# Kernel tuning notes

Hardware: AMD Instinct MI355X
Metric: run time of the kernel (lower is better)

Reference implementation:

```python
import jax, jax.numpy as jnp
import numpy as np

EMBED_DIM = 1024
N_HEADS = 16
HEAD_DIM = EMBED_DIM // N_HEADS
B, T = 1, 4096

def setup_inputs() -> dict:
    key = jax.random.key(0)
    k1, k2, k3 = jax.random.split(key, 3)
    x = jax.random.normal(k1, (B, T, EMBED_DIM), dtype=jnp.float32)
    # match nn.Linear init scale roughly (not required for correctness testing)
    w_qkv = jax.random.normal(k2, (EMBED_DIM, 3 * EMBED_DIM), dtype=jnp.float32) * (EMBED_DIM ** -0.5)
    w_out = jax.random.normal(k3, (EMBED_DIM, EMBED_DIM), dtype=jnp.float32) * (EMBED_DIM ** -0.5)
    return {"x": x, "w_qkv": w_qkv, "w_out": w_out}

def reference(x, w_qkv, w_out):
    b, t, c = x.shape
    qkv = x @ w_qkv                                  # [B,T,3C]
    q, k, v = jnp.split(qkv, 3, axis=-1)
    # [B,T,C] -> [B,H,T,D]
    def heads(a):
        return a.reshape(b, t, N_HEADS, HEAD_DIM).transpose(0, 2, 1, 3)
    q, k, v = heads(q), heads(k), heads(v)
    scale = 1.0 / jnp.sqrt(jnp.asarray(HEAD_DIM, dtype=x.dtype))
    att = jnp.einsum('bhqd,bhkd->bhqk', q, k) * scale  # [B,H,T,T] (full matrix, as in source)
    att = jax.nn.softmax(att, axis=-1)
    y = jnp.einsum('bhqk,bhkd->bhqd', att, v)          # [B,H,T,D]
    y = y.transpose(0, 2, 1, 3).reshape(b, t, c)
    return y @ w_out
```

## Files before the change

### kernel.cpp

```cpp
#include <hip/hip_runtime.h>
#include <hip/hip_bf16.h>

#define T_SEQ 4096
#define C_DIM 1024
#define NH    16
#define HD    64
#define C3    3072

typedef __attribute__((ext_vector_type(8))) short short8;
typedef __attribute__((ext_vector_type(4))) short short4v;
typedef __attribute__((ext_vector_type(4))) float f32x4;
typedef __attribute__((ext_vector_type(16))) float f32x16;

__device__ __forceinline__ short f2bf(float f) {
  union { float f; unsigned u; } v; v.f = f;
  unsigned r = v.u + 0x7FFFu + ((v.u >> 16) & 1u);
  return (short)(r >> 16);
}

__device__ __forceinline__ unsigned cvt_pk_bf16(float lo, float hi) {
  unsigned r;
  asm volatile("v_cvt_pk_bf16_f32 %0, %1, %2" : "=v"(r) : "v"(lo), "v"(hi));
  return r;
}

__device__ __forceinline__ float exp2_fast(float x) {
  return __builtin_amdgcn_exp2f(x);
}

__device__ __forceinline__ float max_half64(float v) {
  return fmaxf(v, __shfl_xor(v, 32, 64));
}

__device__ __forceinline__ float m3(float a, float b, float c) {
  return fmaxf(fmaxf(a, b), c);
}

__device__ __forceinline__ void gld_lds16(const void* g, void* l) {
  __builtin_amdgcn_global_load_lds(
      (const __attribute__((address_space(1))) unsigned int*)g,
      (__attribute__((address_space(3))) unsigned int*)l, 16, 0, 0);
}

__global__ __launch_bounds__(256) void conv_bf16_kernel(const float* __restrict__ in,
                                                        short* __restrict__ out) {
  const size_t i = ((size_t)blockIdx.x * 256 + threadIdx.x) * 8;
  float4 v0 = *(const float4*)(in + i);
  float4 v1 = *(const float4*)(in + i + 4);
  short8 o;
  o[0] = f2bf(v0.x); o[1] = f2bf(v0.y); o[2] = f2bf(v0.z); o[3] = f2bf(v0.w);
  o[4] = f2bf(v1.x); o[5] = f2bf(v1.y); o[6] = f2bf(v1.z); o[7] = f2bf(v1.w);
  *(short8*)(out + i) = o;
}

__global__ void trans_conv2_kernel(const float* __restrict__ wq, short* __restrict__ wqT,
                                   const float* __restrict__ wo, short* __restrict__ woT) {
  const float* in;
  short* out;
  int N, bx = blockIdx.x;
  if (bx < C3 / 32) { in = wq; out = wqT; N = C3; }
  else              { in = wo; out = woT; N = C_DIM; bx -= C3 / 32; }
  const int K = C_DIM;
  __shared__ float t[32][33];
  const int n0 = bx * 32, k0 = blockIdx.y * 32;
  const int tx = threadIdx.x, ty = threadIdx.y;
  for (int i = ty; i < 32; i += 8) t[i][tx] = in[(size_t)(k0 + i) * N + n0 + tx];
  __syncthreads();
  for (int i = ty; i < 32; i += 8) out[(size_t)(n0 + i) * K + k0 + tx] = f2bf(t[tx][i]);
}

__global__ __launch_bounds__(256) void gemm_bt_kernel(const short* __restrict__ A,
                                                      const short* __restrict__ BT,
                                                      short* __restrict__ C,
                                                      short* __restrict__ vTout,
                                                      int vcol0,
                                                      int M, int N, int K) {
  __shared__ __align__(16) short As[128 * 32];
  __shared__ __align__(16) short Bs[128 * 32];
  const int tid = threadIdx.x;
  const int wid = tid >> 6;
  const int lane = tid & 63;
  const int l15 = lane & 15;
  const int l4 = lane >> 4;
  const int wr = wid >> 1;
  const int wc = wid & 1;

  const int nwg = gridDim.x * gridDim.y;
  int lin = blockIdx.y * gridDim.x + blockIdx.x;
  lin = (lin & 7) * (nwg >> 3) + (lin >> 3);
  const int bm = (lin / gridDim.x) * 128;
  const int bn = (lin % gridDim.x) * 128;

  f32x4 acc[4][4];
#pragma unroll
  for (int m = 0; m < 4; ++m)
#pragma unroll
    for (int n = 0; n < 4; ++n) acc[m][n] = (f32x4){0.f, 0.f, 0.f, 0.f};

  const int ebase = wid * 1024;
  const int e0 = ebase + lane * 8;
  const int r0 = e0 >> 5, c0 = e0 & 31;
  const int r1 = r0 + 16;

  for (int k0 = 0; k0 < K; k0 += 32) {
    __syncthreads();
    gld_lds16(A + (size_t)(bm + r0) * K + k0 + c0, As + ebase);
    gld_lds16(A + (size_t)(bm + r1) * K + k0 + c0, As + ebase + 512);
    gld_lds16(BT + (size_t)(bn + r0) * K + k0 + c0, Bs + ebase);
    gld_lds16(BT + (size_t)(bn + r1) * K + k0 + c0, Bs + ebase + 512);
    __syncthreads();

    short8 a[4], b[4];
#pragma unroll
    for (int m = 0; m < 4; ++m)
      a[m] = *(const short8*)&As[(wr * 64 + m * 16 + l15) * 32 + l4 * 8];
#pragma unroll
    for (int n = 0; n < 4; ++n)
      b[n] = *(const short8*)&Bs[(wc * 64 + n * 16 + l15) * 32 + l4 * 8];
#pragma unroll
    for (int m = 0; m < 4; ++m)
#pragma unroll
      for (int n = 0; n < 4; ++n)
        acc[m][n] = __builtin_amdgcn_mfma_f32_16x16x32_bf16(a[m], b[n], acc[m][n], 0, 0, 0);
  }

  if (bn >= vcol0) {
#pragma unroll
    for (int m = 0; m < 4; ++m) {
      const int row0 = bm + wr * 64 + m * 16 + l4 * 4;
#pragma unroll
      for (int n = 0; n < 4; ++n) {
        const int col = bn + wc * 64 + n * 16 + l15;
        short4v o;
#pragma unroll
        for (int r = 0; r < 4; ++r) o[r] = f2bf(acc[m][n][r]);
        *(short4v*)&vTout[(size_t)(col - vcol0) * M + row0] = o;
      }
    }
  } else {
#pragma unroll
    for (int m = 0; m < 4; ++m) {
      const int row0 = bm + wr * 64 + m * 16 + l4 * 4;
#pragma unroll
      for (int n = 0; n < 4; ++n) {
        const int col = bn + wc * 64 + n * 16 + l15;
#pragma unroll
        for (int r = 0; r < 4; ++r)
          C[(size_t)(row0 + r) * N + col] = f2bf(acc[m][n][r]);
      }
    }
  }
}

__global__ __launch_bounds__(256) void gemm_bt64_kernel(const short* __restrict__ A,
                                                        const short* __restrict__ BT,
                                                        float* __restrict__ C,
                                                        int M, int N, int K) {
  __shared__ __align__(16) short As[128 * 32];
  __shared__ __align__(16) short Bs[64 * 32];
  const int tid = threadIdx.x;
  const int wid = tid >> 6;
  const int lane = tid & 63;
  const int l15 = lane & 15;
  const int l4 = lane >> 4;
  const int wr = wid >> 1;
  const int wc = wid & 1;

  const int nwg = gridDim.x * gridDim.y;
  int lin = blockIdx.y * gridDim.x + blockIdx.x;
  lin = (lin & 7) * (nwg >> 3) + (lin >> 3);
  const int bm = (lin / gridDim.x) * 128;
  const int bn = (lin % gridDim.x) * 64;

  f32x4 acc[4][2];
#pragma unroll
  for (int m = 0; m < 4; ++m)
#pragma unroll
    for (int n = 0; n < 2; ++n) acc[m][n] = (f32x4){0.f, 0.f, 0.f, 0.f};

  const int ebase = wid * 1024;
  const int e0 = ebase + lane * 8;
  const int r0 = e0 >> 5, c0 = e0 & 31;
  const int r1 = r0 + 16;
  const int eb = wid * 512 + lane * 8;
  const int rb = eb >> 5, cb = eb & 31;

  for (int k0 = 0; k0 < K; k0 += 32) {
    __syncthreads();
    gld_lds16(A + (size_t)(bm + r0) * K + k0 + c0, As + ebase);
    gld_lds16(A + (size_t)(bm + r1) * K + k0 + c0, As + ebase + 512);
    gld_lds16(BT + (size_t)(bn + rb) * K + k0 + cb, Bs + eb);
    __syncthreads();

    short8 a[4], b[2];
#pragma unroll
    for (int m = 0; m < 4; ++m)
      a[m] = *(const short8*)&As[(wr * 64 + m * 16 + l15) * 32 + l4 * 8];
#pragma unroll
    for (int n = 0; n < 2; ++n)
      b[n] = *(const short8*)&Bs[(wc * 32 + n * 16 + l15) * 32 + l4 * 8];
#pragma unroll
    for (int m = 0; m < 4; ++m)
#pragma unroll
      for (int n = 0; n < 2; ++n)
        acc[m][n] = __builtin_amdgcn_mfma_f32_16x16x32_bf16(a[m], b[n], acc[m][n], 0, 0, 0);
  }

#pragma unroll
  for (int m = 0; m < 4; ++m) {
    const int row0 = bm + wr * 64 + m * 16 + l4 * 4;
#pragma unroll
    for (int n = 0; n < 2; ++n) {
      const int col = bn + wc * 32 + n * 16 + l15;
#pragma unroll
      for (int r = 0; r < 4; ++r)
        C[(size_t)(row0 + r) * N + col] = acc[m][n][r];
    }
  }
}

__global__ __launch_bounds__(256, 2) void attn_kernel(const short* __restrict__ qkv,
                                                      const short* __restrict__ vT,
                                                      short* __restrict__ y) {
  const int bid = blockIdx.x;
  const int xcd = bid & 7, slot = bid >> 3;
  const int h = xcd * 2 + (slot >> 5);
  const int q0 = (slot & 31) * 128;

  const int tid = threadIdx.x;
  const int w = tid >> 6, lane = tid & 63, l31 = lane & 31, l1 = lane >> 5;
  const int g = w >> 1, wg = w & 1;
  const int kvbase = g * (T_SEQ / 2);

  __shared__ __align__(16) short SM[17408];

  short8 qfA[4], qfB[4];
  {
    const short* qp = qkv + (size_t)(q0 + wg * 64 + l31) * C3 + h * 64 + l1 * 8;
#pragma unroll
    for (int ks = 0; ks < 4; ++ks) {
      qfA[ks] = *(const short8*)(qp + ks * 16);
      qfB[ks] = *(const short8*)(qp + (size_t)32 * C3 + ks * 16);
    }
  }

  f32x16 oaA0, oaA1, oaB0, oaB1;
#pragma unroll
  for (int r = 0; r < 16; ++r) { oaA0[r] = 0.f; oaA1[r] = 0.f; oaB0[r] = 0.f; oaB1[r] = 0.f; }
  float mA = -INFINITY, lA = 0.f, mB = -INFINITY, lB = 0.f;
  const float SCL = 0.125f * 1.44269504f;
  const float TH = 8.0f / SCL;

  const int csw = ((lane & 7) << 3) ^ ((lane >> 3) << 3);
  const short* kpt = qkv + 1024 + h * 64 + csw +
                     (size_t)(kvbase + wg * 16 + (lane >> 3)) * C3;
  const int lu = (lane & 7) ^ (lane >> 3);
  const short* vpt = vT + (size_t)(h * 64 + wg * 16 + (lane >> 3) + (lu >> 2) * 32) * T_SEQ +
                     kvbase + (lu & 3) * 8;
  const int rswz = (l31 & 7) << 3;

  short* const Kbase = SM + g * 4096;
  short* const Vbase = SM + 8192 + g * 4096;

  auto stage = [&](int buf) {
#pragma unroll
    for (int i = 0; i < 2; ++i) {
      gld_lds16(kpt + (size_t)i * 8 * C3, Kbase + buf * 2048 + wg * 1024 + i * 512);
      gld_lds16(vpt + (size_t)i * 8 * T_SEQ, Vbase + buf * 2048 + wg * 1024 + i * 512);
    }
  };

  stage(0);
  kpt += (size_t)32 * C3;
  vpt += 32;

  const int NT = (T_SEQ / 2) / 32;
  for (int t = 0; t < NT; ++t) {
    const int cur = t & 1;
    __builtin_amdgcn_s_barrier();
    if (t + 1 < NT) {
      stage(cur ^ 1);
      kpt += (size_t)32 * C3;
      vpt += 32;
      asm volatile("s_waitcnt vmcnt(4)" ::: "memory");
    } else {
      asm volatile("s_waitcnt vmcnt(0)" ::: "memory");
    }
    __builtin_amdgcn_s_barrier();

    const short* Kb = Kbase + cur * 2048;
    const short* Vb = Vbase + cur * 2048;

    f32x16 sA, sB;
#pragma unroll
    for (int r = 0; r < 16; ++r) { sA[r] = 0.f; sB[r] = 0.f; }
    __builtin_amdgcn_s_setprio(1);
#pragma unroll
    for (int ks = 0; ks < 4; ++ks) {
      const int c = (ks * 16 + l1 * 8) ^ rswz;
      short8 kf = *(const short8*)&Kb[l31 * 64 + c];
      sA = __builtin_amdgcn_mfma_f32_32x32x16_bf16(kf, qfA[ks], sA, 0, 0, 0);
      sB = __builtin_amdgcn_mfma_f32_32x32x16_bf16(kf, qfB[ks], sB, 0, 0, 0);
    }
    __builtin_amdgcn_s_setprio(0);

    float tmA, tmB;
    {
      float v0 = m3(sA[0], sA[1], sA[2]);
      float v1 = m3(sA[3], sA[4], sA[5]);
      float v2 = m3(sA[6], sA[7], sA[8]);
      float v3 = m3(sA[9], sA[10], sA[11]);
      float v4 = m3(sA[12], sA[13], sA[14]);
      tmA = fmaxf(m3(v0, v1, v2), m3(v3, v4, sA[15]));
      float u0 = m3(sB[0], sB[1], sB[2]);
      float u1 = m3(sB[3], sB[4], sB[5]);
      float u2 = m3(sB[6], sB[7], sB[8]);
      float u3 = m3(sB[9], sB[10], sB[11]);
      float u4 = m3(sB[12], sB[13], sB[14]);
      tmB = fmaxf(m3(u0, u1, u2), m3(u3, u4, sB[15]));
    }

    if (__any(fmaxf(tmA - mA, tmB - mB) > TH)) {
      const float txA = max_half64(tmA);
      const float mnA = fmaxf(mA, txA);
      const float alA = exp2_fast((mA - mnA) * SCL);
      mA = mnA; lA *= alA;
      const float txB = max_half64(tmB);
      const float mnB = fmaxf(mB, txB);
      const float alB = exp2_fast((mB - mnB) * SCL);
      mB = mnB; lB *= alB;
#pragma unroll
      for (int r = 0; r < 16; ++r) {
        oaA0[r] *= alA; oaA1[r] *= alA;
        oaB0[r] *= alB; oaB1[r] *= alB;
      }
    }
    const float mscA = mA * SCL, mscB = mB * SCL;
#pragma unroll
    for (int r = 0; r < 16; ++r) sA[r] = exp2_fast(fmaf(sA[r], SCL, -mscA));
#pragma unroll
    for (int r = 0; r < 16; ++r) sB[r] = exp2_fast(fmaf(sB[r], SCL, -mscB));

    {
      float u[8];
#pragma unroll
      for (int r = 0; r < 8; ++r) u[r] = sA[r] + sA[r + 8];
#pragma unroll
      for (int r = 0; r < 4; ++r) u[r] += u[r + 4];
      lA += (u[0] + u[2]) + (u[1] + u[3]);
#pragma unroll
      for (int r = 0; r < 8; ++r) u[r] = sB[r] + sB[r + 8];
#pragma unroll
      for (int r = 0; r < 4; ++r) u[r] += u[r + 4];
      lB += (u[0] + u[2]) + (u[1] + u[3]);
    }

    unsigned pwA[2][4], pwB[2][4];
#pragma unroll
    for (int kh = 0; kh < 2; ++kh) {
      {
        unsigned x0 = cvt_pk_bf16(sA[kh * 8 + 0], sA[kh * 8 + 1]);
        unsigned y0 = cvt_pk_bf16(sA[kh * 8 + 4], sA[kh * 8 + 5]);
        asm volatile("s_nop 0\n\tv_permlane32_swap_b32 %0, %1" : "+v"(x0), "+v"(y0));
        unsigned x1 = cvt_pk_bf16(sA[kh * 8 + 2], sA[kh * 8 + 3]);
        unsigned y1 = cvt_pk_bf16(sA[kh * 8 + 6], sA[kh * 8 + 7]);
        asm volatile("s_nop 0\n\tv_permlane32_swap_b32 %0, %1" : "+v"(x1), "+v"(y1));
        pwA[kh][0] = x0; pwA[kh][1] = x1; pwA[kh][2] = y0; pwA[kh][3] = y1;
      }
      {
        unsigned x0 = cvt_pk_bf16(sB[kh * 8 + 0], sB[kh * 8 + 1]);
        unsigned y0 = cvt_pk_bf16(sB[kh * 8 + 4], sB[kh * 8 + 5]);
        asm volatile("s_nop 0\n\tv_permlane32_swap_b32 %0, %1" : "+v"(x0), "+v"(y0));
        unsigned x1 = cvt_pk_bf16(sB[kh * 8 + 2], sB[kh * 8 + 3]);
        unsigned y1 = cvt_pk_bf16(sB[kh * 8 + 6], sB[kh * 8 + 7]);
        asm volatile("s_nop 0\n\tv_permlane32_swap_b32 %0, %1" : "+v"(x1), "+v"(y1));
        pwB[kh][0] = x0; pwB[kh][1] = x1; pwB[kh][2] = y0; pwB[kh][3] = y1;
      }
    }

    __builtin_amdgcn_s_setprio(1);
#pragma unroll
    for (int kh = 0; kh < 2; ++kh) {
      union { unsigned u[4]; short8 s8; } ua, ub;
      ua.u[0] = pwA[kh][0]; ua.u[1] = pwA[kh][1]; ua.u[2] = pwA[kh][2]; ua.u[3] = pwA[kh][3];
      ub.u[0] = pwB[kh][0]; ub.u[1] = pwB[kh][1]; ub.u[2] = pwB[kh][2]; ub.u[3] = pwB[kh][3];
      {
        const int unit = ((0 * 4 + kh * 2 + l1) ^ (l31 & 7));
        short8 vf = *(const short8*)&Vb[l31 * 64 + unit * 8];
        oaA0 = __builtin_amdgcn_mfma_f32_32x32x16_bf16(vf, ua.s8, oaA0, 0, 0, 0);
        oaB0 = __builtin_amdgcn_mfma_f32_32x32x16_bf16(vf, ub.s8, oaB0, 0, 0, 0);
      }
      {
        const int unit = ((1 * 4 + kh * 2 + l1) ^ (l31 & 7));
        short8 vf = *(const short8*)&Vb[l31 * 64 + unit * 8];
        oaA1 = __builtin_amdgcn_mfma_f32_32x32x16_bf16(vf, ua.s8, oaA1, 0, 0, 0);
        oaB1 = __builtin_amdgcn_mfma_f32_32x32x16_bf16(vf, ub.s8, oaB1, 0, 0, 0);
      }
    }
    __builtin_amdgcn_s_setprio(0);
  }

  lA += __shfl_xor(lA, 32, 64);
  lB += __shfl_xor(lB, 32, 64);

  __syncthreads();
  float* Oex = (float*)SM;
  float* mex = ((float*)SM) + 8192;
  if (g == 1) {
    float* ob = Oex + wg * 4096;
#pragma unroll
    for (int r = 0; r < 16; ++r) {
      ob[r * 64 + lane] = oaA0[r];
      ob[(16 + r) * 64 + lane] = oaA1[r];
      ob[(32 + r) * 64 + lane] = oaB0[r];
      ob[(48 + r) * 64 + lane] = oaB1[r];
    }
    float4 ml = {mA, lA, mB, lB};
    *(float4*)&mex[wg * 256 + lane * 4] = ml;
  }
  __syncthreads();
  if (g == 0) {
    const float4 ml = *(const float4*)&mex[wg * 256 + lane * 4];
    const float* ob = Oex + wg * 4096;
    {
      const float mm = fmaxf(mA, ml.x);
      const float a = exp2_fast((mA - mm) * SCL);
      const float b = exp2_fast((ml.x - mm) * SCL);
      const float rl = 1.0f / (lA * a + ml.y * b);
      const float ra = a * rl, rb = b * rl;
      const size_t yb = (size_t)(q0 + wg * 64 + l31) * C_DIM + h * 64;
#pragma unroll
      for (int g4 = 0; g4 < 4; ++g4) {
        short4v o0, o1;
#pragma unroll
        for (int j = 0; j < 4; ++j) {
          o0[j] = f2bf(oaA0[g4 * 4 + j] * ra + ob[(g4 * 4 + j) * 64 + lane] * rb);
          o1[j] = f2bf(oaA1[g4 * 4 + j] * ra + ob[(16 + g4 * 4 + j) * 64 + lane] * rb);
        }
        *(short4v*)&y[yb + g4 * 8 + l1 * 4] = o0;
        *(short4v*)&y[yb + 32 + g4 * 8 + l1 * 4] = o1;
      }
    }
    {
      const float mm = fmaxf(mB, ml.z);
      const float a = exp2_fast((mB - mm) * SCL);
      const float b = exp2_fast((ml.z - mm) * SCL);
      const float rl = 1.0f / (lB * a + ml.w * b);
      const float ra = a * rl, rb = b * rl;
      const size_t yb = (size_t)(q0 + wg * 64 + 32 + l31) * C_DIM + h * 64;
#pragma unroll
      for (int g4 = 0; g4 < 4; ++g4) {
        short4v o0, o1;
#pragma unroll
        for (int j = 0; j < 4; ++j) {
          o0[j] = f2bf(oaB0[g4 * 4 + j] * ra + ob[(32 + g4 * 4 + j) * 64 + lane] * rb);
          o1[j] = f2bf(oaB1[g4 * 4 + j] * ra + ob[(48 + g4 * 4 + j) * 64 + lane] * rb);
        }
        *(short4v*)&y[yb + g4 * 8 + l1 * 4] = o0;
        *(short4v*)&y[yb + 32 + g4 * 8 + l1 * 4] = o1;
      }
    }
  }
}

extern "C" void kernel_launch(void* const* d_in, const int* in_sizes, int n_in,
                              void* d_out, int out_size, void* d_ws, size_t ws_size,
                              hipStream_t stream) {
  const float* x = (const float*)d_in[0];
  const float* w_qkv = (const float*)d_in[1];
  const float* w_out = (const float*)d_in[2];
  float* out = (float*)d_out;

  char* ws = (char*)d_ws;
  short* xb = (short*)ws;            ws += (size_t)T_SEQ * C_DIM * 2;
  short* wqT = (short*)ws;           ws += (size_t)C3 * C_DIM * 2;
  short* woT = (short*)ws;           ws += (size_t)C_DIM * C_DIM * 2;
  short* qkv = (short*)ws;           ws += (size_t)T_SEQ * C3 * 2;
  short* vT = (short*)ws;            ws += (size_t)NH * T_SEQ * HD * 2;
  short* y = (short*)ws;             ws += (size_t)T_SEQ * C_DIM * 2;

  conv_bf16_kernel<<<(T_SEQ * C_DIM) / (256 * 8), 256, 0, stream>>>(x, xb);
  trans_conv2_kernel<<<dim3(C3 / 32 + C_DIM / 32, C_DIM / 32), dim3(32, 8), 0, stream>>>(
      w_qkv, wqT, w_out, woT);

  gemm_bt_kernel<<<dim3(C3 / 128, T_SEQ / 128), 256, 0, stream>>>(xb, wqT, qkv, vT, 2048,
                                                                  T_SEQ, C3, C_DIM);

  attn_kernel<<<512, 256, 0, stream>>>(qkv, vT, y);

  gemm_bt64_kernel<<<dim3(C_DIM / 64, T_SEQ / 128), 256, 0, stream>>>(y, woT, out,
                                                                      T_SEQ, C_DIM, C_DIM);
}
```

Before: 164.7 us.

## Split attention KV range across four wave groups with tree merge

Doubles the attention block to 512 threads so four wave-group pairs each process a quarter of the key/value sequence instead of half. Partial softmax states are combined through shared memory in a two-level reduction before normalization and store. This shortens each wave's serial KV loop and raises waves per CU, at the cost of doubled LDS per block, extra barriers and merge work, and the launch bound of 4 may pressure registers.

```diff
diff --git a/kernel.cpp b/kernel.cpp
--- a/kernel.cpp
+++ b/kernel.cpp
@@ -219,7 +219,7 @@
   }
 }
 
-__global__ __launch_bounds__(256, 2) void attn_kernel(const short* __restrict__ qkv,
+__global__ __launch_bounds__(512, 4) void attn_kernel(const short* __restrict__ qkv,
                                                       const short* __restrict__ vT,
                                                       short* __restrict__ y) {
   const int bid = blockIdx.x;
@@ -230,9 +230,9 @@
   const int tid = threadIdx.x;
   const int w = tid >> 6, lane = tid & 63, l31 = lane & 31, l1 = lane >> 5;
   const int g = w >> 1, wg = w & 1;
-  const int kvbase = g * (T_SEQ / 2);
-
-  __shared__ __align__(16) short SM[17408];
+  const int kvbase = g * (T_SEQ / 4);
+
+  __shared__ __align__(16) short SM[34816];
 
   short8 qfA[4], qfB[4];
   {
@@ -260,7 +260,7 @@
   const int rswz = (l31 & 7) << 3;
 
   short* const Kbase = SM + g * 4096;
-  short* const Vbase = SM + 8192 + g * 4096;
+  short* const Vbase = SM + 16384 + g * 4096;
 
   auto stage = [&](int buf) {
 #pragma unroll
@@ -274,7 +274,7 @@
   kpt += (size_t)32 * C3;
   vpt += 32;
 
-  const int NT = (T_SEQ / 2) / 32;
+  const int NT = (T_SEQ / 4) / 32;
   for (int t = 0; t < NT; ++t) {
     const int cur = t & 1;
     __builtin_amdgcn_s_barrier();
@@ -403,11 +403,11 @@
   lA += __shfl_xor(lA, 32, 64);
   lB += __shfl_xor(lB, 32, 64);
 
-  __syncthreads();
   float* Oex = (float*)SM;
-  float* mex = ((float*)SM) + 8192;
-  if (g == 1) {
-    float* ob = Oex + wg * 4096;
+  float* mex = ((float*)SM) + 16384;
+
+  auto writeSlot = [&](int s) {
+    float* ob = Oex + s * 4096;
 #pragma unroll
     for (int r = 0; r < 16; ++r) {
       ob[r * 64 + lane] = oaA0[r];
@@ -416,49 +416,64 @@
       ob[(48 + r) * 64 + lane] = oaB1[r];
     }
     float4 ml = {mA, lA, mB, lB};
-    *(float4*)&mex[wg * 256 + lane * 4] = ml;
-  }
-  __syncthreads();
-  if (g == 0) {
-    const float4 ml = *(const float4*)&mex[wg * 256 + lane * 4];
-    const float* ob = Oex + wg * 4096;
+    *(float4*)&mex[s * 256 + lane * 4] = ml;
+  };
+  auto mergeSlot = [&](int s) {
+    const float4 ml = *(const float4*)&mex[s * 256 + lane * 4];
+    const float* ob = Oex + s * 4096;
     {
       const float mm = fmaxf(mA, ml.x);
       const float a = exp2_fast((mA - mm) * SCL);
       const float b = exp2_fast((ml.x - mm) * SCL);
-      const float rl = 1.0f / (lA * a + ml.y * b);
-      const float ra = a * rl, rb = b * rl;
-      const size_t yb = (size_t)(q0 + wg * 64 + l31) * C_DIM + h * 64;
-#pragma unroll
-      for (int g4 = 0; g4 < 4; ++g4) {
-        short4v o0, o1;
-#pragma unroll
-        for (int j = 0; j < 4; ++j) {
-          o0[j] = f2bf(oaA0[g4 * 4 + j] * ra + ob[(g4 * 4 + j) * 64 + lane] * rb);
-          o1[j] = f2bf(oaA1[g4 * 4 + j] * ra + ob[(16 + g4 * 4 + j) * 64 + lane] * rb);
-        }
-        *(short4v*)&y[yb + g4 * 8 + l1 * 4] = o0;
-        *(short4v*)&y[yb + 32 + g4 * 8 + l1 * 4] = o1;
+      mA = mm; lA = lA * a + ml.y * b;
+#pragma unroll
+      for (int r = 0; r < 16; ++r) {
+        oaA0[r] = oaA0[r] * a + ob[r * 64 + lane] * b;
+        oaA1[r] = oaA1[r] * a + ob[(16 + r) * 64 + lane] * b;
       }
     }
     {
       const float mm = fmaxf(mB, ml.z);
       const float a = exp2_fast((mB - mm) * SCL);
       const float b = exp2_fast((ml.z - mm) * SCL);
-      const float rl = 1.0f / (lB * a + ml.w * b);
-      const float ra = a * rl, rb = b * rl;
-      const size_t yb = (size_t)(q0 + wg * 64 + 32 + l31) * C_DIM + h * 64;
-#pragma unroll
-      for (int g4 = 0; g4 < 4; ++g4) {
-        short4v o0, o1;
-#pragma unroll
-        for (int j = 0; j < 4; ++j) {
-          o0[j] = f2bf(oaB0[g4 * 4 + j] * ra + ob[(32 + g4 * 4 + j) * 64 + lane] * rb);
-          o1[j] = f2bf(oaB1[g4 * 4 + j] * ra + ob[(48 + g4 * 4 + j) * 64 + lane] * rb);
-        }
-        *(short4v*)&y[yb + g4 * 8 + l1 * 4] = o0;
-        *(short4v*)&y[yb + 32 + g4 * 8 + l1 * 4] = o1;
-      }
+      mB = mm; lB = lB * a + ml.w * b;
+#pragma unroll
+      for (int r = 0; r < 16; ++r) {
+        oaB0[r] = oaB0[r] * a + ob[(32 + r) * 64 + lane] * b;
+        oaB1[r] = oaB1[r] * a + ob[(48 + r) * 64 + lane] * b;
+      }
+    }
+  };
+
+  __syncthreads();
+  if (g == 1) writeSlot(wg * 2 + 0);
+  if (g == 3) writeSlot(wg * 2 + 1);
+  __syncthreads();
+  if (g == 0) mergeSlot(wg * 2 + 0);
+  if (g == 2) mergeSlot(wg * 2 + 1);
+  __syncthreads();
+  if (g == 2) writeSlot(wg * 2 + 0);
+  __syncthreads();
+  if (g == 0) {
+    mergeSlot(wg * 2 + 0);
+    const float rlA = 1.0f / lA;
+    const float rlB = 1.0f / lB;
+    const size_t ybA = (size_t)(q0 + wg * 64 + l31) * C_DIM + h * 64;
+    const size_t ybB = (size_t)(q0 + wg * 64 + 32 + l31) * C_DIM + h * 64;
+#pragma unroll
+    for (int g4 = 0; g4 < 4; ++g4) {
+      short4v oA0, oA1, oB0, oB1;
+#pragma unroll
+      for (int j = 0; j < 4; ++j) {
+        oA0[j] = f2bf(oaA0[g4 * 4 + j] * rlA);
+        oA1[j] = f2bf(oaA1[g4 * 4 + j] * rlA);
+        oB0[j] = f2bf(oaB0[g4 * 4 + j] * rlB);
+        oB1[j] = f2bf(oaB1[g4 * 4 + j] * rlB);
+      }
+      *(short4v*)&y[ybA + g4 * 8 + l1 * 4] = oA0;
+      *(short4v*)&y[ybA + 32 + g4 * 8 + l1 * 4] = oA1;
+      *(short4v*)&y[ybB + g4 * 8 + l1 * 4] = oB0;
+      *(short4v*)&y[ybB + 32 + g4 * 8 + l1 * 4] = oB1;
     }
   }
 }
@@ -486,7 +501,7 @@
   gemm_bt_kernel<<<dim3(C3 / 128, T_SEQ / 128), 256, 0, stream>>>(xb, wqT, qkv, vT, 2048,
                                                                   T_SEQ, C3, C_DIM);
 
-  attn_kernel<<<512, 256, 0, stream>>>(qkv, vT, y);
+  attn_kernel<<<512, 512, 0, stream>>>(qkv, vT, y);
 
   gemm_bt64_kernel<<<dim3(C_DIM / 64, T_SEQ / 128), 256, 0, stream>>>(y, woT, out,
                                                                       T_SEQ, C_DIM, C_DIM);
```

New measurement: 304.7 us. 1.85x slower.
